# Optimization experiments

Hardware: AMD Instinct MI355X
Metric: run time of the kernel (lower is better)

The kernel has to match this reference:

```python
import jax, jax.numpy as jnp
import numpy as np

# ViT-B/16 CLIP visual tower dims
B, R, P = 32, 224, 16          # batch, resolution, patch
D, H, F, L = 768, 12, 3072, 12 # width, heads, mlp dim, layers
S = 1 + (R // P) ** 2          # 197 tokens (cls + patches)
O = 512                        # output proj dim
HD = D // H
MEAN = jnp.array([0.48145466, 0.4578275, 0.40821073], jnp.float32).reshape(1, 3, 1, 1)
STD = jnp.array([0.26862954, 0.26130258, 0.27577711], jnp.float32).reshape(1, 3, 1, 1)


def _ln(x, s, b):
    m = x.mean(-1, keepdims=True)
    v = ((x - m) ** 2).mean(-1, keepdims=True)
    return (x - m) * jax.lax.rsqrt(v + 1e-5) * s + b


def setup_inputs() -> dict:
    key = jax.random.key(0)
    ks = jax.random.split(key, 16)
    r = lambda i, shape: jax.random.normal(ks[i], shape, jnp.float32) * 0.02
    return dict(
        images=jax.random.uniform(ks[0], (B, 3, R, R), jnp.float32),
        conv_w=r(1, (D, 3, P, P)),
        cls_emb=r(2, (D,)),
        pos_emb=r(3, (S, D)),
        ln_pre_s=jnp.ones((D,), jnp.float32), ln_pre_b=jnp.zeros((D,), jnp.float32),
        ln1_s=jnp.ones((L, D), jnp.float32), ln1_b=jnp.zeros((L, D), jnp.float32),
        qkv_w=r(4, (L, 3 * D, D)), qkv_b=r(5, (L, 3 * D)),
        out_w=r(6, (L, D, D)), out_b=r(7, (L, D)),
        ln2_s=jnp.ones((L, D), jnp.float32), ln2_b=jnp.zeros((L, D), jnp.float32),
        fc_w=r(8, (L, F, D)), fc_b=r(9, (L, F)),
        proj_w=r(10, (L, D, F)), proj_b=r(11, (L, D)),
        ln_post_s=jnp.ones((D,), jnp.float32), ln_post_b=jnp.zeros((D,), jnp.float32),
        vis_proj=r(12, (D, O)),
    )


def reference(images, conv_w, cls_emb, pos_emb, ln_pre_s, ln_pre_b,
              ln1_s, ln1_b, qkv_w, qkv_b, out_w, out_b, ln2_s, ln2_b,
              fc_w, fc_b, proj_w, proj_b, ln_post_s, ln_post_b, vis_proj):
    x = (images - MEAN) / STD
    # conv1 patch embedding (no bias in CLIP): [B,D,14,14]
    x = jax.lax.conv_general_dilated(x, conv_w, (P, P), 'VALID',
                                     dimension_numbers=('NCHW', 'OIHW', 'NCHW'))
    x = x.reshape(B, D, -1).transpose(0, 2, 1)  # [B, 196, D]
    x = jnp.concatenate([jnp.broadcast_to(cls_emb, (B, 1, D)), x], axis=1) + pos_emb
    x = _ln(x, ln_pre_s, ln_pre_b)
    scale = HD ** -0.5

    def block(x, p):
        l1s, l1b, qw, qb, ow, ob, l2s, l2b, fw, fb, pw, pb = p
        h = _ln(x, l1s, l1b)
        qkv = h @ qw.T + qb                      # fused in_proj, [B,S,3D]
        q, k, v = jnp.split(qkv, 3, axis=-1)
        split = lambda t: t.reshape(B, S, H, HD).transpose(0, 2, 1, 3)
        q, k, v = split(q) * scale, split(k), split(v)
        attn = jax.nn.softmax(jnp.einsum('bhqd,bhkd->bhqk', q, k), axis=-1)
        o = jnp.einsum('bhqk,bhkd->bhqd', attn, v).transpose(0, 2, 1, 3).reshape(B, S, D)
        x = x + o @ ow.T + ob                    # out_proj + residual
        h = _ln(x, l2s, l2b) @ fw.T + fb
        h = h * jax.nn.sigmoid(1.702 * h)        # QuickGELU
        x = x + h @ pw.T + pb
        return x, None

    x, _ = jax.lax.scan(block, x, (ln1_s, ln1_b, qkv_w, qkv_b, out_w, out_b,
                                   ln2_s, ln2_b, fc_w, fc_b, proj_w, proj_b))
    x = _ln(x[:, 0], ln_post_s, ln_post_b)  # ln_post on cls token
    return x @ vis_proj                      # [B, 512]
```

## Files before the change

### kernel.cpp

```cpp
#include <hip/hip_runtime.h>
#include <cstddef>

#define Bv   32
#define Sv   197
#define Dv   768
#define Hh   12
#define HDv  64
#define Fv   3072
#define Lv   12
#define Ov   512
#define TOK  (Bv * Sv)
#define MPAD 6400
#define NPATCH 196
#define CONV_M (Bv * NPATCH)

#define WQ_SZ (2304 * 768)
#define WO_SZ (768 * 768)
#define WF_SZ (3072 * 768)
#define WP_SZ (768 * 3072)
#define WTOT  (WQ_SZ + WO_SZ + WF_SZ + WP_SZ)

typedef __attribute__((ext_vector_type(8))) __bf16 bf16x8;
typedef __attribute__((ext_vector_type(4))) float f32x4;

__device__ __forceinline__ unsigned short f2bf(float f) {
    unsigned int u = __float_as_uint(f);
    unsigned int r = (u + 0x7fffu + ((u >> 16) & 1u)) >> 16;
    return (unsigned short)r;
}

__device__ __forceinline__ void async_ld16(const void* g, void* l) {
    __builtin_amdgcn_global_load_lds(
        (__attribute__((address_space(1))) void*)(g),
        (__attribute__((address_space(3))) void*)(l),
        16, 0, 0);
}

__device__ __forceinline__ void reduce2_256(float& s1, float& s2) {
    #pragma unroll
    for (int off = 32; off > 0; off >>= 1) {
        s1 += __shfl_down(s1, off, 64);
        s2 += __shfl_down(s2, off, 64);
    }
    __shared__ float r1[4], r2[4];
    int lane = threadIdx.x & 63, w = threadIdx.x >> 6;
    if (lane == 0) { r1[w] = s1; r2[w] = s2; }
    __syncthreads();
    s1 = r1[0] + r1[1] + r1[2] + r1[3];
    s2 = r2[0] + r2[1] + r2[2] + r2[3];
    __syncthreads();
}

__global__ void convert_kernel(const float* __restrict__ src,
                               unsigned short* __restrict__ dst, int n4) {
    int gid = blockIdx.x * 256 + threadIdx.x;
    if (gid >= n4) return;
    int idx = gid * 4;
    float4 v = *(const float4*)(src + idx);
    ushort4 r = make_ushort4(f2bf(v.x), f2bf(v.y), f2bf(v.z), f2bf(v.w));
    *(ushort4*)(dst + idx) = r;
}

__global__ void convertw_kernel(const float* __restrict__ wq,
                                const float* __restrict__ wo,
                                const float* __restrict__ wf,
                                const float* __restrict__ wp,
                                unsigned short* __restrict__ dst) {
    int idx = (blockIdx.x * 256 + threadIdx.x) * 4;
    const float* s; int off;
    if (idx < WQ_SZ)                     { s = wq; off = idx; }
    else if (idx < WQ_SZ + WO_SZ)        { s = wo; off = idx - WQ_SZ; }
    else if (idx < WQ_SZ + WO_SZ + WF_SZ){ s = wf; off = idx - WQ_SZ - WO_SZ; }
    else                                 { s = wp; off = idx - WQ_SZ - WO_SZ - WF_SZ; }
    float4 v = *(const float4*)(s + off);
    ushort4 r = make_ushort4(f2bf(v.x), f2bf(v.y), f2bf(v.z), f2bf(v.w));
    *(ushort4*)(dst + idx) = r;
}

__global__ void im2col_kernel(const float* __restrict__ img,
                              unsigned short* __restrict__ out) {
    int idx = blockIdx.x * 256 + threadIdx.x;
    int col = idx % 768;
    int row = idx / 768;
    int b = row / NPATCH, p = row % NPATCH;
    int ph = p / 14, pw = p % 14;
    int c  = col >> 8;
    int r  = col & 255;
    int kh = r >> 4, kw = r & 15;
    int y = ph * 16 + kh, x = pw * 16 + kw;
    const float mean[3] = {0.48145466f, 0.4578275f, 0.40821073f};
    const float stdv[3] = {0.26862954f, 0.26130258f, 0.27577711f};
    float v = img[((size_t)(b * 3 + c) * 224 + y) * 224 + x];
    out[idx] = f2bf((v - mean[c]) / stdv[c]);
}

template<int ODT, int ACT>
__global__ __launch_bounds__(512) void gemm_mfma(
        const unsigned short* __restrict__ A, const unsigned short* __restrict__ W,
        const float* __restrict__ bias, const float* __restrict__ res,
        void* __restrict__ Cv, int M, int N, int K)
{
    __shared__ unsigned short As[2][256 * 64];
    __shared__ unsigned short Ws[2][128 * 64];
    const int tid = threadIdx.x;
    const int w = tid >> 6, l = tid & 63;

    const int gx = gridDim.x;
    const int wg  = blockIdx.y * gx + blockIdx.x;
    const int nwg = gx * gridDim.y;
    const int q = nwg >> 3, r8 = nwg & 7;
    const int xcd = wg & 7, lo = wg >> 3;
    const int swz = (xcd < r8 ? xcd * (q + 1) : r8 * (q + 1) + (xcd - r8) * q) + lo;
    const int m0 = (swz / gx) << 8;
    const int n0 = (swz % gx) << 7;

    const int lrow = l >> 3;
    const int lchk = (l & 7) ^ lrow;
    const unsigned short* agp = A + (size_t)(m0 + w * 8 + lrow) * K + lchk * 8;
    const unsigned short* wgp = W + (size_t)(n0 + w * 8 + lrow) * K + lchk * 8;
    const int lbase = (w * 8) * 64;

    const int wm = w >> 1, wn = w & 1;
    const int fr = l & 15, fq = l >> 4;
    int aoff[2][4], woff[2][4];
    #pragma unroll
    for (int ks = 0; ks < 2; ks++) {
        const int pc = ((ks * 4 + fq) ^ (fr & 7)) * 8;
        #pragma unroll
        for (int i = 0; i < 4; i++) {
            aoff[ks][i] = (wm * 64 + i * 16 + fr) * 64 + pc;
            woff[ks][i] = (wn * 64 + i * 16 + fr) * 64 + pc;
        }
    }

    f32x4 acc[4][4] = {};
    const int nt = K >> 6;

    #define STAGE(t, bf) do {                                              \
        const int _ko = (t) << 6;                                          \
        _Pragma("unroll")                                                  \
        for (int _i = 0; _i < 4; _i++)                                     \
            async_ld16(agp + (size_t)_i * 64 * K + _ko,                    \
                       &As[bf][lbase + _i * 64 * 64]);                     \
        _Pragma("unroll")                                                  \
        for (int _i = 0; _i < 2; _i++)                                     \
            async_ld16(wgp + (size_t)_i * 64 * K + _ko,                    \
                       &Ws[bf][lbase + _i * 64 * 64]);                     \
    } while (0)

    auto compute = [&](const unsigned short* ab, const unsigned short* wb) {
        #pragma unroll
        for (int ks = 0; ks < 2; ks++) {
            bf16x8 af[4], wf[4];
            #pragma unroll
            for (int i = 0; i < 4; i++) {
                af[i] = *(const bf16x8*)(ab + aoff[ks][i]);
                wf[i] = *(const bf16x8*)(wb + woff[ks][i]);
            }
            #pragma unroll
            for (int i = 0; i < 4; i++) {
                #pragma unroll
                for (int j = 0; j < 4; j++) {
                    acc[i][j] = __builtin_amdgcn_mfma_f32_16x16x32_bf16(
                        af[i], wf[j], acc[i][j], 0, 0, 0);
                }
            }
        }
    };

    STAGE(0, 0);
    asm volatile("s_waitcnt vmcnt(0)" ::: "memory");
    __builtin_amdgcn_s_barrier();

    int bf = 0;
    for (int t = 0; t < nt; t++) {
        if (t + 1 < nt) STAGE(t + 1, bf ^ 1);
        compute(As[bf], Ws[bf]);
        if (t + 1 < nt) {
            asm volatile("s_waitcnt vmcnt(0)" ::: "memory");
            __builtin_amdgcn_s_barrier();
            bf ^= 1;
        }
    }
    #undef STAGE

    float bn[4];
    #pragma unroll
    for (int j = 0; j < 4; j++)
        bn[j] = bias ? bias[n0 + wn * 64 + j * 16 + fr] : 0.f;

    #pragma unroll
    for (int i = 0; i < 4; i++) {
        #pragma unroll
        for (int r = 0; r < 4; r++) {
            int m = m0 + wm * 64 + i * 16 + fq * 4 + r;
            if (m < M) {
                size_t rowb = (size_t)m * N;
                #pragma unroll
                for (int j = 0; j < 4; j++) {
                    int n = n0 + wn * 64 + j * 16 + fr;
                    float v = acc[i][j][r] + bn[j];
                    if (res) v += res[rowb + n];
                    if (ACT) v = v / (1.f + __expf(-1.702f * v));
                    if (ODT == 0) ((float*)Cv)[rowb + n] = v;
                    else ((unsigned short*)Cv)[rowb + n] = f2bf(v);
                }
            }
        }
    }
}

__global__ void ln_kernel(const float* __restrict__ in, unsigned short* __restrict__ out,
                          const float* __restrict__ s, const float* __restrict__ b) {
    int t = blockIdx.x;
    const float* row = in + (size_t)t * Dv;
    int tid = threadIdx.x;
    float v[3], s1 = 0.f, s2 = 0.f;
    #pragma unroll
    for (int i = 0; i < 3; i++) {
        v[i] = row[tid + 256 * i];
        s1 += v[i]; s2 += v[i] * v[i];
    }
    reduce2_256(s1, s2);
    float mean = s1 * (1.0f / Dv);
    float var  = s2 * (1.0f / Dv) - mean * mean;
    float rstd = rsqrtf(var + 1e-5f);
    unsigned short* orow = out + (size_t)t * Dv;
    #pragma unroll
    for (int i = 0; i < 3; i++) {
        int d = tid + 256 * i;
        orow[d] = f2bf((v[i] - mean) * rstd * s[d] + b[d]);
    }
}

__global__ void embed_ln_kernel(const float* __restrict__ conv_out,
                                const float* __restrict__ cls,
                                const float* __restrict__ pos,
                                const float* __restrict__ s,
                                const float* __restrict__ b,
                                float* __restrict__ x) {
    int t = blockIdx.x;
    int bb = t / Sv, si = t % Sv;
    int tid = threadIdx.x;
    float v[3], s1 = 0.f, s2 = 0.f;
    #pragma unroll
    for (int i = 0; i < 3; i++) {
        int d = tid + 256 * i;
        float e = (si == 0) ? cls[d]
                            : conv_out[((size_t)bb * NPATCH + (si - 1)) * Dv + d];
        v[i] = e + pos[(size_t)si * Dv + d];
        s1 += v[i]; s2 += v[i] * v[i];
    }
    reduce2_256(s1, s2);
    float mean = s1 * (1.0f / Dv);
    float var  = s2 * (1.0f / Dv) - mean * mean;
    float rstd = rsqrtf(var + 1e-5f);
    float* orow = x + (size_t)t * Dv;
    #pragma unroll
    for (int i = 0; i < 3; i++) {
        int d = tid + 256 * i;
        orow[d] = (v[i] - mean) * rstd * s[d] + b[d];
    }
}

__global__ __launch_bounds__(256) void attn4_kernel(
        const unsigned short* __restrict__ qkv, unsigned short* __restrict__ o) {
    const int qg = blockIdx.x, h = blockIdx.y, b = blockIdx.z;
    __shared__ __align__(16) unsigned short vt[64][232];
    __shared__ __align__(16) unsigned short pb[32][236];
    __shared__ float red[4][32];
    __shared__ float smax_f[32];
    __shared__ float sinv_f[32];

    const int tid = threadIdx.x;
    const int w = tid >> 6, l = tid & 63;
    const int fr = l & 15, fq = l >> 4;
    const size_t base = (size_t)b * Sv;
    const unsigned int* q32 = (const unsigned int*)qkv;

    for (int i = tid; i < 224 * 32; i += 256) {
        int j = i >> 5, u = i & 31;
        unsigned int val = (j < Sv) ? q32[(base + j) * 1152 + 768 + h * 32 + u] : 0u;
        vt[2 * u][j]     = (unsigned short)(val & 0xffffu);
        vt[2 * u + 1][j] = (unsigned short)(val >> 16);
    }

    union U { uint4 u; bf16x8 v; };

    f32x4 sc[2][4] = {};
    #pragma unroll
    for (int ks = 0; ks < 2; ks++) {
        U aq[2];
        #pragma unroll
        for (int mt = 0; mt < 2; mt++) {
            int row = qg * 32 + mt * 16 + fr;
            int rc = row < Sv ? row : Sv - 1;
            aq[mt].u = *(const uint4*)(qkv + (base + rc) * 2304 + h * 64 + ks * 32 + fq * 8);
        }
        #pragma unroll
        for (int s = 0; s < 4; s++) {
            int nt = w + 4 * s;
            if (nt >= 14) continue;
            int col = nt * 16 + fr;
            int cc = col < Sv ? col : Sv - 1;
            U bq;
            bq.u = *(const uint4*)(qkv + (base + cc) * 2304 + 768 + h * 64 + ks * 32 + fq * 8);
            #pragma unroll
            for (int mt = 0; mt < 2; mt++)
                sc[mt][s] = __builtin_amdgcn_mfma_f32_16x16x32_bf16(
                    aq[mt].v, bq.v, sc[mt][s], 0, 0, 0);
        }
    }

    float rmax[2][4];
    #pragma unroll
    for (int mt = 0; mt < 2; mt++)
        #pragma unroll
        for (int r = 0; r < 4; r++) rmax[mt][r] = -1e30f;
    #pragma unroll
    for (int mt = 0; mt < 2; mt++) {
        #pragma unroll
        for (int s = 0; s < 4; s++) {
            int nt = w + 4 * s;
            int col = nt * 16 + fr;
            bool valid = (nt < 14) && (col < Sv);
            #pragma unroll
            for (int r = 0; r < 4; r++) {
                float v = valid ? sc[mt][s][r] * 0.125f : -1e30f;
                sc[mt][s][r] = v;
                rmax[mt][r] = fmaxf(rmax[mt][r], v);
            }
        }
    }
    #pragma unroll
    for (int mt = 0; mt < 2; mt++) {
        #pragma unroll
        for (int r = 0; r < 4; r++) {
            float m = rmax[mt][r];
            m = fmaxf(m, __shfl_xor(m, 1, 64));
            m = fmaxf(m, __shfl_xor(m, 2, 64));
            m = fmaxf(m, __shfl_xor(m, 4, 64));
            m = fmaxf(m, __shfl_xor(m, 8, 64));
            rmax[mt][r] = m;
        }
    }
    if (fr == 0) {
        #pragma unroll
        for (int mt = 0; mt < 2; mt++)
            #pragma unroll
            for (int r = 0; r < 4; r++)
                red[w][mt * 16 + fq * 4 + r] = rmax[mt][r];
    }
    __syncthreads();
    if (tid < 32)
        smax_f[tid] = fmaxf(fmaxf(red[0][tid], red[1][tid]),
                            fmaxf(red[2][tid], red[3][tid]));
    __syncthreads();

    float rsum[2][4] = {};
    #pragma unroll
    for (int mt = 0; mt < 2; mt++) {
        float fm[4];
        #pragma unroll
        for (int r = 0; r < 4; r++) fm[r] = smax_f[mt * 16 + fq * 4 + r];
        #pragma unroll
        for (int s = 0; s < 4; s++) {
            int nt = w + 4 * s;
            if (nt >= 14) continue;
            int col = nt * 16 + fr;
            #pragma unroll
            for (int r = 0; r < 4; r++) {
                float p = (col < Sv) ? __expf(sc[mt][s][r] - fm[r]) : 0.f;
                rsum[mt][r] += p;
                pb[mt * 16 + fq * 4 + r][col] = f2bf(p);
            }
        }
    }
    #pragma unroll
    for (int mt = 0; mt < 2; mt++) {
        #pragma unroll
        for (int r = 0; r < 4; r++) {
            float s = rsum[mt][r];
            s += __shfl_xor(s, 1, 64);
            s += __shfl_xor(s, 2, 64);
            s += __shfl_xor(s, 4, 64);
            s += __shfl_xor(s, 8, 64);
            rsum[mt][r] = s;
        }
    }
    if (fr == 0) {
        #pragma unroll
        for (int mt = 0; mt < 2; mt++)
            #pragma unroll
            for (int r = 0; r < 4; r++)
                red[w][mt * 16 + fq * 4 + r] = rsum[mt][r];
    }
    __syncthreads();
    if (tid < 32)
        sinv_f[tid] = 1.f / (red[0][tid] + red[1][tid] + red[2][tid] + red[3][tid]);
    __syncthreads();

    f32x4 oc[2] = {};
    #pragma unroll
    for (int ks = 0; ks < 7; ks++) {
        U bv;
        bv.u = *(const uint4*)&vt[w * 16 + fr][ks * 32 + fq * 8];
        #pragma unroll
        for (int mt = 0; mt < 2; mt++) {
            const unsigned short* ap = &pb[mt * 16 + fr][ks * 32 + fq * 8];
            uint2 lo = *(const uint2*)ap;
            uint2 hi = *(const uint2*)(ap + 4);
            U a; a.u = make_uint4(lo.x, lo.y, hi.x, hi.y);
            oc[mt] = __builtin_amdgcn_mfma_f32_16x16x32_bf16(a.v, bv.v, oc[mt], 0, 0, 0);
        }
    }

    #pragma unroll
    for (int mt = 0; mt < 2; mt++) {
        #pragma unroll
        for (int r = 0; r < 4; r++) {
            int lrow = mt * 16 + fq * 4 + r;
            int row = qg * 32 + lrow;
            if (row < Sv)
                o[(base + row) * Dv + h * 64 + w * 16 + fr] =
                    f2bf(oc[mt][r] * sinv_f[lrow]);
        }
    }
}

__global__ void head_kernel(const float* __restrict__ x,
                            const float* __restrict__ s, const float* __restrict__ b,
                            const float* __restrict__ vp, float* __restrict__ out) {
    int bb = blockIdx.x, tid = threadIdx.x;
    __shared__ float xn[Dv];
    const float* row = x + (size_t)(bb * Sv) * Dv;
    float v[3], s1 = 0.f, s2 = 0.f;
    #pragma unroll
    for (int i = 0; i < 3; i++) {
        v[i] = row[tid + 256 * i];
        s1 += v[i]; s2 += v[i] * v[i];
    }
    reduce2_256(s1, s2);
    float mean = s1 * (1.0f / Dv);
    float var  = s2 * (1.0f / Dv) - mean * mean;
    float rstd = rsqrtf(var + 1e-5f);
    #pragma unroll
    for (int i = 0; i < 3; i++) {
        int d = tid + 256 * i;
        xn[d] = (v[i] - mean) * rstd * s[d] + b[d];
    }
    __syncthreads();
    float acc0 = 0.f, acc1 = 0.f;
    for (int d = 0; d < Dv; d++) {
        float xv = xn[d];
        acc0 += xv * vp[(size_t)d * Ov + tid];
        acc1 += xv * vp[(size_t)d * Ov + tid + 256];
    }
    out[(size_t)bb * Ov + tid]       = acc0;
    out[(size_t)bb * Ov + tid + 256] = acc1;
}

extern "C" void kernel_launch(void* const* d_in, const int* in_sizes, int n_in,
                              void* d_out, int out_size, void* d_ws, size_t ws_size,
                              hipStream_t stream) {
    const float* images   = (const float*)d_in[0];
    const float* conv_w   = (const float*)d_in[1];
    const float* cls_emb  = (const float*)d_in[2];
    const float* pos_emb  = (const float*)d_in[3];
    const float* lnpre_s  = (const float*)d_in[4];
    const float* lnpre_b  = (const float*)d_in[5];
    const float* ln1_s    = (const float*)d_in[6];
    const float* ln1_b    = (const float*)d_in[7];
    const float* qkv_w    = (const float*)d_in[8];
    const float* qkv_b    = (const float*)d_in[9];
    const float* out_w    = (const float*)d_in[10];
    const float* out_b    = (const float*)d_in[11];
    const float* ln2_s    = (const float*)d_in[12];
    const float* ln2_b    = (const float*)d_in[13];
    const float* fc_w     = (const float*)d_in[14];
    const float* fc_b     = (const float*)d_in[15];
    const float* proj_w   = (const float*)d_in[16];
    const float* proj_b   = (const float*)d_in[17];
    const float* lnpost_s = (const float*)d_in[18];
    const float* lnpost_b = (const float*)d_in[19];
    const float* vis_proj = (const float*)d_in[20];
    float* out = (float*)d_out;

    char* p = (char*)d_ws;
    float* x              = (float*)p;          p += (size_t)TOK * Dv * 4;
    unsigned short* abuf  = (unsigned short*)p; p += (size_t)MPAD * Dv * 2;
    unsigned short* qkvb  = (unsigned short*)p; p += (size_t)MPAD * 2304 * 2;
    unsigned short* hbuf  = (unsigned short*)p; p += (size_t)MPAD * Fv * 2;
    unsigned short* wbuf  = (unsigned short*)p; p += (size_t)WTOT * 2;
    unsigned short* cwb   = (unsigned short*)p; p += (size_t)WO_SZ * 2;
    unsigned short* im2c  = qkvb;
    float* convo          = (float*)hbuf;

    const int GY = MPAD / 256;

    convert_kernel<<<WO_SZ / 4 / 256, 256, 0, stream>>>(conv_w, cwb, WO_SZ / 4);
    im2col_kernel<<<(CONV_M * Dv) / 256, 256, 0, stream>>>(images, im2c);
    gemm_mfma<0, 0><<<dim3(Dv / 128, GY), 512, 0, stream>>>(
        im2c, cwb, nullptr, nullptr, convo, CONV_M, Dv, Dv);
    embed_ln_kernel<<<TOK, 256, 0, stream>>>(convo, cls_emb, pos_emb,
                                             lnpre_s, lnpre_b, x);

    unsigned short* wq = wbuf;
    unsigned short* wo = wbuf + WQ_SZ;
    unsigned short* wf = wbuf + WQ_SZ + WO_SZ;
    unsigned short* wp = wbuf + WQ_SZ + WO_SZ + WF_SZ;

    for (int l = 0; l < Lv; l++) {
        convertw_kernel<<<WTOT / 4 / 256, 256, 0, stream>>>(
            qkv_w + (size_t)l * WQ_SZ, out_w + (size_t)l * WO_SZ,
            fc_w + (size_t)l * WF_SZ, proj_w + (size_t)l * WP_SZ, wbuf);
        ln_kernel<<<TOK, 256, 0, stream>>>(x, abuf, ln1_s + l * Dv, ln1_b + l * Dv);
        gemm_mfma<1, 0><<<dim3(2304 / 128, GY), 512, 0, stream>>>(
            abuf, wq, qkv_b + (size_t)l * 2304, nullptr, qkvb, TOK, 2304, Dv);
        attn4_kernel<<<dim3(7, Hh, Bv), 256, 0, stream>>>(qkvb, abuf);
        gemm_mfma<0, 0><<<dim3(Dv / 128, GY), 512, 0, stream>>>(
            abuf, wo, out_b + (size_t)l * Dv, x, x, TOK, Dv, Dv);
        ln_kernel<<<TOK, 256, 0, stream>>>(x, abuf, ln2_s + l * Dv, ln2_b + l * Dv);
        gemm_mfma<1, 1><<<dim3(Fv / 128, GY), 512, 0, stream>>>(
            abuf, wf, fc_b + (size_t)l * Fv, nullptr, hbuf, TOK, Fv, Dv);
        gemm_mfma<0, 0><<<dim3(Dv / 128, GY), 512, 0, stream>>>(
            hbuf, wp, proj_b + (size_t)l * Dv, x, x, TOK, Dv, Fv);
    }

    head_kernel<<<Bv, 256, 0, stream>>>(x, lnpost_s, lnpost_b, vis_proj, out);
}
```

Before: 4.255 ms.

## Shrink GEMM tiles to 128x128 and split-K the residual projections with atomics

```diff
diff --git a/kernel.cpp b/kernel.cpp
--- a/kernel.cpp
+++ b/kernel.cpp
@@ -95,12 +95,12 @@
 }
 
 template<int ODT, int ACT>
-__global__ __launch_bounds__(512) void gemm_mfma(
+__global__ __launch_bounds__(256) void gemm_mfma(
         const unsigned short* __restrict__ A, const unsigned short* __restrict__ W,
         const float* __restrict__ bias, const float* __restrict__ res,
         void* __restrict__ Cv, int M, int N, int K)
 {
-    __shared__ unsigned short As[2][256 * 64];
+    __shared__ unsigned short As[2][128 * 64];
     __shared__ unsigned short Ws[2][128 * 64];
     const int tid = threadIdx.x;
     const int w = tid >> 6, l = tid & 63;
@@ -111,14 +111,17 @@
     const int q = nwg >> 3, r8 = nwg & 7;
     const int xcd = wg & 7, lo = wg >> 3;
     const int swz = (xcd < r8 ? xcd * (q + 1) : r8 * (q + 1) + (xcd - r8) * q) + lo;
-    const int m0 = (swz / gx) << 8;
+    const int m0 = (swz / gx) << 7;
     const int n0 = (swz % gx) << 7;
+
+    const int kseg  = K / gridDim.z;
+    const int kbase = blockIdx.z * kseg;
 
     const int lrow = l >> 3;
     const int lchk = (l & 7) ^ lrow;
-    const unsigned short* agp = A + (size_t)(m0 + w * 8 + lrow) * K + lchk * 8;
-    const unsigned short* wgp = W + (size_t)(n0 + w * 8 + lrow) * K + lchk * 8;
-    const int lbase = (w * 8) * 64;
+    const unsigned short* agp = A + (size_t)(m0 + w * 32 + lrow) * K + kbase + lchk * 8;
+    const unsigned short* wgp = W + (size_t)(n0 + w * 32 + lrow) * K + kbase + lchk * 8;
+    const int lbase = w * 32 * 64;
 
     const int wm = w >> 1, wn = w & 1;
     const int fr = l & 15, fq = l >> 4;
@@ -134,18 +137,18 @@
     }
 
     f32x4 acc[4][4] = {};
-    const int nt = K >> 6;
+    const int nt = kseg >> 6;
 
     #define STAGE(t, bf) do {                                              \
         const int _ko = (t) << 6;                                          \
         _Pragma("unroll")                                                  \
         for (int _i = 0; _i < 4; _i++)                                     \
-            async_ld16(agp + (size_t)_i * 64 * K + _ko,                    \
-                       &As[bf][lbase + _i * 64 * 64]);                     \
+            async_ld16(agp + (size_t)_i * 8 * K + _ko,                     \
+                       &As[bf][lbase + _i * 512]);                         \
         _Pragma("unroll")                                                  \
-        for (int _i = 0; _i < 2; _i++)                                     \
-            async_ld16(wgp + (size_t)_i * 64 * K + _ko,                    \
-                       &Ws[bf][lbase + _i * 64 * 64]);                     \
+        for (int _i = 0; _i < 4; _i++)                                     \
+            async_ld16(wgp + (size_t)_i * 8 * K + _ko,                     \
+                       &Ws[bf][lbase + _i * 512]);                         \
     } while (0)
 
     auto compute = [&](const unsigned short* ab, const unsigned short* wb) {
@@ -169,25 +172,22 @@
     };
 
     STAGE(0, 0);
-    asm volatile("s_waitcnt vmcnt(0)" ::: "memory");
-    __builtin_amdgcn_s_barrier();
+    __syncthreads();
 
     int bf = 0;
     for (int t = 0; t < nt; t++) {
         if (t + 1 < nt) STAGE(t + 1, bf ^ 1);
         compute(As[bf], Ws[bf]);
-        if (t + 1 < nt) {
-            asm volatile("s_waitcnt vmcnt(0)" ::: "memory");
-            __builtin_amdgcn_s_barrier();
-            bf ^= 1;
-        }
+        __syncthreads();
+        bf ^= 1;
     }
     #undef STAGE
 
+    const bool addb = (ODT != 2) || (blockIdx.z == 0);
     float bn[4];
     #pragma unroll
     for (int j = 0; j < 4; j++)
-        bn[j] = bias ? bias[n0 + wn * 64 + j * 16 + fr] : 0.f;
+        bn[j] = (bias && addb) ? bias[n0 + wn * 64 + j * 16 + fr] : 0.f;
 
     #pragma unroll
     for (int i = 0; i < 4; i++) {
@@ -200,10 +200,14 @@
                 for (int j = 0; j < 4; j++) {
                     int n = n0 + wn * 64 + j * 16 + fr;
                     float v = acc[i][j][r] + bn[j];
-                    if (res) v += res[rowb + n];
-                    if (ACT) v = v / (1.f + __expf(-1.702f * v));
-                    if (ODT == 0) ((float*)Cv)[rowb + n] = v;
-                    else ((unsigned short*)Cv)[rowb + n] = f2bf(v);
+                    if (ODT == 2) {
+                        atomicAdd((float*)Cv + rowb + n, v);
+                    } else {
+                        if (res) v += res[rowb + n];
+                        if (ACT) v = v / (1.f + __expf(-1.702f * v));
+                        if (ODT == 0) ((float*)Cv)[rowb + n] = v;
+                        else ((unsigned short*)Cv)[rowb + n] = f2bf(v);
+                    }
                 }
             }
         }
@@ -496,11 +500,11 @@
     unsigned short* im2c  = qkvb;
     float* convo          = (float*)hbuf;
 
-    const int GY = MPAD / 256;
+    const int GY = MPAD / 128;
 
     convert_kernel<<<WO_SZ / 4 / 256, 256, 0, stream>>>(conv_w, cwb, WO_SZ / 4);
     im2col_kernel<<<(CONV_M * Dv) / 256, 256, 0, stream>>>(images, im2c);
-    gemm_mfma<0, 0><<<dim3(Dv / 128, GY), 512, 0, stream>>>(
+    gemm_mfma<0, 0><<<dim3(Dv / 128, GY, 1), 256, 0, stream>>>(
         im2c, cwb, nullptr, nullptr, convo, CONV_M, Dv, Dv);
     embed_ln_kernel<<<TOK, 256, 0, stream>>>(convo, cls_emb, pos_emb,
                                              lnpre_s, lnpre_b, x);
@@ -515,16 +519,16 @@
             qkv_w + (size_t)l * WQ_SZ, out_w + (size_t)l * WO_SZ,
             fc_w + (size_t)l * WF_SZ, proj_w + (size_t)l * WP_SZ, wbuf);
         ln_kernel<<<TOK, 256, 0, stream>>>(x, abuf, ln1_s + l * Dv, ln1_b + l * Dv);
-        gemm_mfma<1, 0><<<dim3(2304 / 128, GY), 512, 0, stream>>>(
+        gemm_mfma<1, 0><<<dim3(2304 / 128, GY, 1), 256, 0, stream>>>(
             abuf, wq, qkv_b + (size_t)l * 2304, nullptr, qkvb, TOK, 2304, Dv);
         attn4_kernel<<<dim3(7, Hh, Bv), 256, 0, stream>>>(qkvb, abuf);
-        gemm_mfma<0, 0><<<dim3(Dv / 128, GY), 512, 0, stream>>>(
-            abuf, wo, out_b + (size_t)l * Dv, x, x, TOK, Dv, Dv);
+        gemm_mfma<2, 0><<<dim3(Dv / 128, GY, 2), 256, 0, stream>>>(
+            abuf, wo, out_b + (size_t)l * Dv, nullptr, x, TOK, Dv, Dv);
         ln_kernel<<<TOK, 256, 0, stream>>>(x, abuf, ln2_s + l * Dv, ln2_b + l * Dv);
-        gemm_mfma<1, 1><<<dim3(Fv / 128, GY), 512, 0, stream>>>(
+        gemm_mfma<1, 1><<<dim3(Fv / 128, GY, 1), 256, 0, stream>>>(
             abuf, wf, fc_b + (size_t)l * Fv, nullptr, hbuf, TOK, Fv, Dv);
-        gemm_mfma<0, 0><<<dim3(Dv / 128, GY), 512, 0, stream>>>(
-            hbuf, wp, proj_b + (size_t)l * Dv, x, x, TOK, Dv, Fv);
+        gemm_mfma<2, 0><<<dim3(Dv / 128, GY, 2), 256, 0, stream>>>(
+            hbuf, wp, proj_b + (size_t)l * Dv, nullptr, x, TOK, Dv, Fv);
     }
 
     head_kernel<<<Bv, 256, 0, stream>>>(x, lnpost_s, lnpost_b, vis_proj, out);
```

Result: faster. 4.135 ms (-2.8%).
